# Optimization experiments

Hardware: AMD Instinct MI355X
Metric: run time of the kernel (lower is better)

Reference implementation:

```python
import jax, jax.numpy as jnp
import numpy as np
import math

# Config constants (match init_kwargs)
E = 8          # n_experts
TOPK = 2       # attn_topk
DIM = 1024     # transformer_dim
B = 4          # batch_size
S = 1024       # max_seq_len
H = 1024       # num_heads * head_dim
SCALE = 1.0 / math.sqrt(DIM)  # original divides scores by sqrt(self.dim)


def setup_inputs() -> dict:
    key = jax.random.key(0)
    ks = jax.random.split(key, 8)
    w = 0.02  # weight init scale
    return {
        "X": jax.random.normal(ks[0], (B, S, DIM), jnp.float32),
        "mask": jnp.ones((B, S), jnp.float32),
        "switch_W": jax.random.normal(ks[1], (DIM * S, E), jnp.float32) * w,
        "switch_b": jnp.zeros((E,), jnp.float32),
        "Wq": jax.random.normal(ks[2], (E, DIM, H), jnp.float32) * w,
        "bq": jnp.zeros((E, H), jnp.float32),
        "Wk": jax.random.normal(ks[3], (E, DIM, H), jnp.float32) * w,
        "bk": jnp.zeros((E, H), jnp.float32),
        "Wv": jax.random.normal(ks[4], (E, DIM, H), jnp.float32) * w,
        "bv": jnp.zeros((E, H), jnp.float32),
        "Wff": jax.random.normal(ks[5], (E, H, DIM), jnp.float32) * w,
        "bff": jnp.zeros((E, DIM), jnp.float32),
    }


def _dispatch_mask(route_prob):
    # top-k expert routing per batch element -> hard {0,1} mask [B, E]
    _, idx = jax.lax.top_k(route_prob, TOPK)  # [B, TOPK]
    b = route_prob.shape[0]
    return jnp.zeros((b, E), route_prob.dtype).at[jnp.arange(b)[:, None], idx].set(1.0)


def reference(X, mask, switch_W, switch_b, Wq, bq, Wk, bk, Wv, bv, Wff, bff):
    b, s, d = X.shape
    # Router: Linear(dim*seq_len -> n_experts) + softmax; preprocess -> idx_list
    logits = X.reshape(b, -1) @ switch_W + switch_b          # [B, E]
    route_prob = jax.nn.softmax(logits, axis=-1)
    m = _dispatch_mask(route_prob)                            # [B, E] dispatch mask (idx_list)

    # Per-expert Q/K/V projections (ColumnParallelLinearWithMoE over routed batches)
    Q = jnp.einsum('bsd,edh->ebsh', X, Wq) + bq[:, None, None, :]  # [E,B,S,H]
    K = jnp.einsum('bsd,edh->ebsh', X, Wk) + bk[:, None, None, :]
    V = jnp.einsum('bsd,edh->ebsh', X, Wv) + bv[:, None, None, :]

    # RowParallelMatmulWithMoE: per-expert scores, softmax (dropout p=0)
    scores = jnp.einsum('ebsh,ebth->ebst', Q, K) * SCALE      # [E,B,S,S]
    P = jax.nn.softmax(scores, axis=-1)

    # index_add_ combine of per-expert attn maps (second preprocess reuses same routing)
    A = jnp.einsum('be,ebst->bst', m, P)                      # [B,S,S]

    # ColumnParallelMatmulWithMoE: attn @ V per expert
    ctx = jnp.einsum('bst,ebth->ebsh', A, V)                  # [E,B,S,H]

    # RowParallelLinearWithMoE output projection, then index_add_ combine
    out = jnp.einsum('ebsh,ehd->ebsd', ctx, Wff) + bff[:, None, None, :]
    y = jnp.einsum('be,ebsd->bsd', m, out)                    # [B,S,DIM]
    return y
```

## Files before the change

kernel.cpp:

```cpp
#include <hip/hip_runtime.h>
#include <math.h>

typedef unsigned short u16;
typedef __attribute__((ext_vector_type(8))) short bffrag;
typedef __attribute__((ext_vector_type(4))) float f32x4;
typedef __attribute__((ext_vector_type(4))) unsigned short us4;
typedef __attribute__((ext_vector_type(8))) unsigned short us8;

#define SCALE_QK (1.0f/32.0f)

__device__ __forceinline__ u16 f2bf(float f) {
    unsigned u = __builtin_bit_cast(unsigned, f);
    u += 0x7fffu + ((u >> 16) & 1u);
    return (u16)(u >> 16);
}
__device__ __forceinline__ float bf2f(u16 v) {
    unsigned u = ((unsigned)v) << 16;
    return __builtin_bit_cast(float, u);
}

__device__ __forceinline__ void gld16(const u16* g, u16* l) {
    __builtin_amdgcn_global_load_lds(
        (const __attribute__((address_space(1))) void*)g,
        (__attribute__((address_space(3))) void*)l, 16, 0, 0);
}

__global__ __launch_bounds__(256) void router_partial(const float* __restrict__ X,
                                                      const float* __restrict__ sW,
                                                      float* __restrict__ part) {
    float acc[32];
    #pragma unroll
    for (int a = 0; a < 32; ++a) acc[a] = 0.f;
    int tid = blockIdx.x * 256 + threadIdx.x;
    #pragma unroll
    for (int q = 0; q < 4; ++q) {
        int i = tid + q * 262144;
        float4 w0 = *(const float4*)(sW + (size_t)i * 8);
        float4 w1 = *(const float4*)(sW + (size_t)i * 8 + 4);
        #pragma unroll
        for (int b = 0; b < 4; ++b) {
            float x = X[((size_t)b << 20) + i];
            acc[b*8+0] += x * w0.x; acc[b*8+1] += x * w0.y;
            acc[b*8+2] += x * w0.z; acc[b*8+3] += x * w0.w;
            acc[b*8+4] += x * w1.x; acc[b*8+5] += x * w1.y;
            acc[b*8+6] += x * w1.z; acc[b*8+7] += x * w1.w;
        }
    }
    __shared__ float wsum[4][32];
    int lane = threadIdx.x & 63, wv = threadIdx.x >> 6;
    #pragma unroll
    for (int a = 0; a < 32; ++a) {
        float v = acc[a];
        #pragma unroll
        for (int off = 32; off; off >>= 1) v += __shfl_down(v, off, 64);
        if (lane == 0) wsum[wv][a] = v;
    }
    __syncthreads();
    int t = threadIdx.x;
    if (t < 32)
        part[(size_t)t * 1024 + blockIdx.x] = wsum[0][t] + wsum[1][t] + wsum[2][t] + wsum[3][t];
}

__global__ __launch_bounds__(256) void router_final(const float* __restrict__ part,
                                                    const float* __restrict__ sb,
                                                    int* __restrict__ sel_need) {
    __shared__ float ps[32][8];
    __shared__ float lg[32];
    int t = threadIdx.x, a = t >> 3, c = t & 7;
    {
        float s = 0.f;
        const float* p = part + (size_t)a * 1024 + c * 128;
        for (int i = 0; i < 128; ++i) s += p[i];
        ps[a][c] = s;
    }
    __syncthreads();
    if (t < 32) {
        float v = 0.f;
        #pragma unroll
        for (int j = 0; j < 8; ++j) v += ps[t][j];
        lg[t] = v + sb[t & 7];
    }
    __syncthreads();
    if (t < 4) {
        int base = t * 8;
        int e1 = 0; float v1 = lg[base];
        for (int e = 1; e < 8; ++e) { if (lg[base + e] > v1) { v1 = lg[base + e]; e1 = e; } }
        int e2 = -1; float v2 = -INFINITY;
        for (int e = 0; e < 8; ++e) {
            if (e == e1) continue;
            if (lg[base + e] > v2) { v2 = lg[base + e]; e2 = e; }
        }
        sel_need[t * 2] = e1; sel_need[t * 2 + 1] = e2;
    }
    __syncthreads();
    if (t < 8) {
        int need = 0;
        for (int j = 0; j < 8; ++j) need |= (sel_need[j] == t);
        sel_need[8 + t] = need;
    }
}

__global__ __launch_bounds__(256) void c1_partial(const float* __restrict__ Wff,
        const float* __restrict__ bv, const int* __restrict__ sel_need,
        float* __restrict__ cpart) {
    int e = blockIdx.z;
    if (!sel_need[8 + e]) return;
    int d = blockIdx.x * 256 + threadIdx.x;
    int h0 = blockIdx.y * 128;
    const float* W = Wff + ((size_t)e << 20) + (size_t)h0 * 1024 + d;
    const float* bvp = bv + e * 1024 + h0;
    float s = 0.f;
    #pragma unroll 4
    for (int h = 0; h < 128; ++h) s += bvp[h] * W[(size_t)h * 1024];
    cpart[(e * 8 + blockIdx.y) * 1024 + d] = s;
}

__global__ __launch_bounds__(256) void ybias_kernel(const float* __restrict__ cpart,
        const float* __restrict__ bff, const int* __restrict__ sel,
        float* __restrict__ ybias) {
    int b = blockIdx.y;
    int d = blockIdx.x * 256 + threadIdx.x;
    int e0 = sel[b * 2], e1 = sel[b * 2 + 1];
    float c0 = 0.f, c1v = 0.f;
    #pragma unroll
    for (int hc = 0; hc < 8; ++hc) {
        c0  += cpart[(e0 * 8 + hc) * 1024 + d];
        c1v += cpart[(e1 * 8 + hc) * 1024 + d];
    }
    ybias[b * 1024 + d] = 2.f * (c0 + c1v) + bff[e0 * 1024 + d] + bff[e1 * 1024 + d];
}

__global__ __launch_bounds__(256) void cvt_all(const float* __restrict__ Wq,
                                               const float* __restrict__ Wk,
                                               const float* __restrict__ Wff,
                                               const float* __restrict__ X,
                                               const float* __restrict__ Wv,
                                               const int* __restrict__ sel_need,
                                               u16* __restrict__ WqT, u16* __restrict__ WkT,
                                               u16* __restrict__ WffT,
                                               u16* __restrict__ Xb, u16* __restrict__ WvB) {
    int z = blockIdx.z;
    int R0 = blockIdx.y * 128, C0 = blockIdx.x * 128;
    int t = threadIdx.x;
    if (z < 24) {
        int type = z >> 3, e = z & 7;
        if (!sel_need[8 + e]) return;
        const float* src = (type == 0 ? Wq : type == 1 ? Wk : Wff) + ((size_t)e << 20);
        u16* dst = (type == 0 ? WqT : type == 1 ? WkT : WffT) + ((size_t)e << 20);
        __shared__ u16 lt[128 * 136];
        int c = t & 127;
        int rh = (t >> 7) * 4;
        #pragma unroll
        for (int it = 0; it < 16; ++it) {
            int r4 = it * 8 + rh;
            us4 o;
            #pragma unroll
            for (int j = 0; j < 4; ++j)
                o[j] = f2bf(src[(size_t)(R0 + r4 + j) * 1024 + C0 + c]);
            *(us4*)&lt[c * 136 + r4] = o;
        }
        __syncthreads();
        int dd = (t & 15) * 8;
        int hh = t >> 4;
        #pragma unroll
        for (int it = 0; it < 8; ++it) {
            int cr = it * 16 + hh;
            us8 o = *(const us8*)&lt[cr * 136 + dd];
            *(us8*)(dst + (size_t)(C0 + cr) * 1024 + R0 + dd) = o;
        }
    } else {
        const float* src; u16* dst;
        if (z < 28) {
            int b = z - 24;
            src = X + ((size_t)b << 20);  dst = Xb + ((size_t)b << 20);
        } else {
            int e = z - 28;
            if (!sel_need[8 + e]) return;
            src = Wv + ((size_t)e << 20);  dst = WvB + ((size_t)e << 20);
        }
        int r = t >> 4;
        int c8 = (t & 15) * 8;
        #pragma unroll
        for (int it = 0; it < 8; ++it) {
            int row = R0 + it * 16 + r;
            const float* sp = src + (size_t)row * 1024 + C0 + c8;
            float4 a = *(const float4*)sp;
            float4 b2 = *(const float4*)(sp + 4);
            us8 o;
            o[0] = f2bf(a.x); o[1] = f2bf(a.y); o[2] = f2bf(a.z); o[3] = f2bf(a.w);
            o[4] = f2bf(b2.x); o[5] = f2bf(b2.y); o[6] = f2bf(b2.z); o[7] = f2bf(b2.w);
            *(us8*)(dst + (size_t)row * 1024 + C0 + c8) = o;
        }
    }
}

__device__ __forceinline__ void stage_half8(const u16* g, int ld, u16* ldst, int tid) {
    int r = tid >> 3;
    int j = ((tid ^ r) & 7) * 8;
    gld16(g + (size_t)r * ld + j, ldst + tid * 8);
    gld16(g + (size_t)(r + 64) * ld + j, ldst + 4096 + tid * 8);
}

template<int Q, bool LASTVM>
__device__ __forceinline__ void phase8(const u16* Ac, const bffrag (&bfr)[4][2],
                                       f32x4 (&acc)[8][4], int rb, int l15, int x0,
                                       const u16* sg, int sld, u16* sdst, int tid) {
    bffrag af[2][2];
    #pragma unroll
    for (int mm = 0; mm < 2; ++mm) {
        int r = (rb + Q * 32 + mm * 16 + l15) * 64;
        af[mm][0] = *(const bffrag*)(Ac + r + x0);
        af[mm][1] = *(const bffrag*)(Ac + r + (x0 ^ 32));
    }
    __builtin_amdgcn_sched_barrier(0);
    stage_half8(sg, sld, sdst, tid);
    __builtin_amdgcn_sched_barrier(0);
    __builtin_amdgcn_s_barrier();
    asm volatile("s_waitcnt lgkmcnt(0)" ::: "memory");
    __builtin_amdgcn_sched_barrier(0);
    __builtin_amdgcn_s_setprio(1);
    #pragma unroll
    for (int ks = 0; ks < 2; ++ks)
        #pragma unroll
        for (int mm = 0; mm < 2; ++mm)
            #pragma unroll
            for (int nn = 0; nn < 4; ++nn)
                acc[Q*2+mm][nn] = __builtin_amdgcn_mfma_f32_16x16x32_bf16(
                    af[mm][ks], bfr[nn][ks], acc[Q*2+mm][nn], 0, 0, 0);
    __builtin_amdgcn_s_setprio(0);
    __builtin_amdgcn_sched_barrier(0);
    if (LASTVM) asm volatile("s_waitcnt vmcnt(4)" ::: "memory");
    __builtin_amdgcn_s_barrier();
}

__device__ __forceinline__ void gemm8(const u16* __restrict__ A, int lda,
                                      const u16* __restrict__ B, int ldb,
                                      int K, f32x4 (&acc)[8][4]) {
    __shared__ u16 lds[65536];
    const int tid = threadIdx.x, l = tid & 63, wid = tid >> 6;
    const int wr = wid >> 2, wc = wid & 3;
    const int l15 = l & 15;
    const int rb = wr * 128;
    const int cb = wc * 64;
    const int x0 = (((l >> 4) ^ (l & 7)) * 8);
    const int m0 = blockIdx.y * 256, n0 = blockIdx.x * 256;
    const int nt = K >> 6;

    const u16* Ag = A + (size_t)m0 * lda;
    const u16* Bg = B + (size_t)n0 * ldb;

    stage_half8(Ag,                          lda, lds,                 tid);
    stage_half8(Ag + (size_t)128 * lda,      lda, lds + 8192,          tid);
    stage_half8(Bg,                          ldb, lds + 16384,         tid);
    stage_half8(Bg + (size_t)128 * ldb,      ldb, lds + 16384 + 8192,  tid);
    stage_half8(Bg + 64,                     ldb, lds + 32768 + 16384, tid);
    stage_half8(Bg + 64 + (size_t)128 * ldb, ldb, lds + 32768 + 16384 + 8192, tid);
    asm volatile("s_waitcnt vmcnt(4)" ::: "memory");
    __builtin_amdgcn_s_barrier();

    for (int t7 = 0; t7 < nt; ++t7) {
        const int cur = t7 & 1;
        u16* Ac = lds + cur * 32768;
        u16* Bc = Ac + 16384;
        u16* An = lds + (cur ^ 1) * 32768;
        const int ka = (t7 + 1 < nt ? t7 + 1 : nt - 1) << 6;
        const int kb = (t7 + 2 < nt ? t7 + 2 : nt - 1) << 6;
        const u16* sA0 = Ag + ka;
        const u16* sA1 = Ag + (size_t)128 * lda + ka;
        const u16* sB0 = Bg + kb;
        const u16* sB1 = Bg + (size_t)128 * ldb + kb;

        bffrag bfr[4][2];
        #pragma unroll
        for (int nn = 0; nn < 4; ++nn) {
            int r = (cb + nn * 16 + l15) * 64;
            bfr[nn][0] = *(const bffrag*)(Bc + r + x0);
            bfr[nn][1] = *(const bffrag*)(Bc + r + (x0 ^ 32));
        }
        phase8<0, false>(Ac, bfr, acc, rb, l15, x0, sA0, lda, An, tid);
        phase8<1, false>(Ac, bfr, acc, rb, l15, x0, sA1, lda, An + 8192, tid);
        phase8<2, false>(Ac, bfr, acc, rb, l15, x0, sB0, ldb, Bc, tid);
        phase8<3, true >(Ac, bfr, acc, rb, l15, x0, sB1, ldb, Bc + 8192, tid);
    }
}

__device__ __forceinline__ void zero8(f32x4 (&acc)[8][4]) {
    #pragma unroll
    for (int m = 0; m < 8; ++m)
        #pragma unroll
        for (int n = 0; n < 4; ++n)
            #pragma unroll
            for (int i = 0; i < 4; ++i) acc[m][n][i] = 0.f;
}

__device__ __forceinline__ void epi8_bf16(u16* __restrict__ C, int ldc, float scale,
                                          const f32x4 (&acc)[8][4],
                                          const float* __restrict__ biasN) {
    const int tid = threadIdx.x, l = tid & 63, wid = tid >> 6;
    const int wr = wid >> 2, wc = wid & 3;
    const int m0 = blockIdx.y * 256 + wr * 128, n0 = blockIdx.x * 256 + wc * 64;
    const int l15 = l & 15, l4 = (l >> 4) * 4;
    #pragma unroll
    for (int mt = 0; mt < 8; ++mt)
        #pragma unroll
        for (int nn = 0; nn < 4; ++nn) {
            int col = n0 + nn * 16 + l15;
            float bn = biasN ? biasN[col] : 0.f;
            #pragma unroll
            for (int i = 0; i < 4; ++i) {
                int row = m0 + mt * 16 + l4 + i;
                C[(size_t)row * ldc + col] = f2bf(acc[mt][nn][i] * scale + bn);
            }
        }
}

__global__ __launch_bounds__(512) void mfma8_qk(const u16* __restrict__ Xb,
        const u16* __restrict__ WqT, const u16* __restrict__ WkT,
        const float* __restrict__ bq, const float* __restrict__ bk,
        const int* __restrict__ sel, u16* __restrict__ Qb, u16* __restrict__ Kb) {
    int z = blockIdx.z, w = z >> 3, bs = z & 7;
    int b = bs >> 1, e = sel[bs];
    f32x4 acc[8][4]; zero8(acc);
    gemm8(Xb + ((size_t)b << 20), 1024, (w ? WkT : WqT) + ((size_t)e << 20), 1024, 1024, acc);
    epi8_bf16((w ? Kb : Qb) + ((size_t)bs << 20), 1024, 1.0f, acc, (w ? bk : bq) + e * 1024);
}

__global__ __launch_bounds__(512) void mfma8_sw(const u16* __restrict__ Qb,
        const u16* __restrict__ Kb, const u16* __restrict__ WffT,
        const u16* __restrict__ WvB, const int* __restrict__ sel,
        u16* __restrict__ Sb, u16* __restrict__ P0b, u16* __restrict__ P1b) {
    int z = blockIdx.z;
    f32x4 acc[8][4]; zero8(acc);
    if (z < 8) {
        gemm8(Qb + ((size_t)z << 20), 1024, Kb + ((size_t)z << 20), 1024, 1024, acc);
        epi8_bf16(Sb + ((size_t)z << 20), 1024, SCALE_QK, acc, nullptr);
    } else {
        int h = (z >= 12), b = z & 3, e = sel[b * 2 + h];
        gemm8(WffT + ((size_t)e << 20), 1024, WvB + ((size_t)e << 20), 1024, 1024, acc);
        epi8_bf16((h ? P1b : P0b) + ((size_t)b << 20), 1024, 1.0f, acc, nullptr);
    }
}

__global__ __launch_bounds__(256) void wvfadd(const u16* __restrict__ P0b,
                                              const u16* __restrict__ P1b,
                                              u16* __restrict__ W) {
    size_t i = (size_t)(blockIdx.x * 256 + threadIdx.x) * 8;
    us8 a = *(const us8*)(P0b + i);
    us8 b = *(const us8*)(P1b + i);
    us8 o;
    #pragma unroll
    for (int j = 0; j < 8; ++j) o[j] = f2bf(bf2f(a[j]) + bf2f(b[j]));
    *(us8*)(W + i) = o;
}

__device__ __forceinline__ void stage_tile(const u16* a0, const u16* a1,
                                           const u16* b0, const u16* b1,
                                           u16* sa, u16* sb, int tid) {
    gld16(a0, &sa[tid * 8]);
    gld16(a1, &sa[2048 + tid * 8]);
    gld16(b0, &sb[tid * 8]);
    gld16(b1, &sb[2048 + tid * 8]);
}

__device__ __forceinline__ void gemm_ds(const u16* __restrict__ A, int lda,
                                        const u16* __restrict__ B, int ldb,
                                        int K, int m0, int n0, f32x4 (&acc)[4][4]) {
    __shared__ u16 sA[2][4096];
    __shared__ u16 sB[2][4096];
    const int tid = threadIdx.x, lane = tid & 63, wv = tid >> 6;
    const int wr = (wv >> 1) * 64, wc = (wv & 1) * 64;
    const int l15 = lane & 15, lk = (lane >> 4) * 8;
    const int r0 = tid >> 2, k8 = (tid & 3) * 8;

    const u16* a0 = A + (size_t)(m0 + r0) * lda + k8;
    const u16* a1 = A + (size_t)(m0 + 64 + r0) * lda + k8;
    const u16* b0 = B + (size_t)(n0 + r0) * ldb + k8;
    const u16* b1 = B + (size_t)(n0 + 64 + r0) * ldb + k8;

    stage_tile(a0, a1, b0, b1, sA[0], sB[0], tid);
    __syncthreads();

    const int nt = K >> 5;
    for (int t = 0; t < nt; ++t) {
        const int cur = t & 1;
        if (t + 1 < nt) {
            int k0 = (t + 1) << 5;
            stage_tile(a0 + k0, a1 + k0, b0 + k0, b1 + k0, sA[cur ^ 1], sB[cur ^ 1], tid);
        }
        bffrag av[4], bf[4];
        #pragma unroll
        for (int m = 0; m < 4; ++m)
            av[m] = *reinterpret_cast<const bffrag*>(&sA[cur][(wr + m * 16 + l15) * 32 + lk]);
        #pragma unroll
        for (int n = 0; n < 4; ++n)
            bf[n] = *reinterpret_cast<const bffrag*>(&sB[cur][(wc + n * 16 + l15) * 32 + lk]);
        #pragma unroll
        for (int m = 0; m < 4; ++m)
            #pragma unroll
            for (int n = 0; n < 4; ++n)
                acc[m][n] = __builtin_amdgcn_mfma_f32_16x16x32_bf16(av[m], bf[n], acc[m][n], 0, 0, 0);
        __syncthreads();
    }
}

__device__ __forceinline__ void zero_acc(f32x4 (&acc)[4][4]) {
    #pragma unroll
    for (int m = 0; m < 4; ++m)
        #pragma unroll
        for (int n = 0; n < 4; ++n)
            #pragma unroll
            for (int i = 0; i < 4; ++i) acc[m][n][i] = 0.f;
}

__device__ __forceinline__ void epi4_bf16(u16* __restrict__ C, int ldc, int m0, int n0,
                                          const f32x4 (&acc)[4][4]) {
    const int tid = threadIdx.x, lane = tid & 63, wv = tid >> 6;
    const int wr = (wv >> 1) * 64, wc = (wv & 1) * 64;
    const int l15 = lane & 15, l4 = (lane >> 4) * 4;
    #pragma unroll
    for (int m = 0; m < 4; ++m)
        #pragma unroll
        for (int n = 0; n < 4; ++n) {
            int col = n0 + wc + n * 16 + l15;
            #pragma unroll
            for (int i = 0; i < 4; ++i) {
                int row = m0 + wr + m * 16 + l4 + i;
                C[(size_t)row * ldc + col] = f2bf(acc[m][n][i]);
            }
        }
}

__device__ __forceinline__ void epi4_f32(float* __restrict__ C, int ldc, int m0, int n0,
                                         const f32x4 (&acc)[4][4],
                                         const float* __restrict__ bias1) {
    const int tid = threadIdx.x, lane = tid & 63, wv = tid >> 6;
    const int wr = (wv >> 1) * 64, wc = (wv & 1) * 64;
    const int l15 = lane & 15, l4 = (lane >> 4) * 4;
    #pragma unroll
    for (int m = 0; m < 4; ++m)
        #pragma unroll
        for (int n = 0; n < 4; ++n) {
            int col = n0 + wc + n * 16 + l15;
            float bn = bias1 ? bias1[col] : 0.f;
            #pragma unroll
            for (int i = 0; i < 4; ++i) {
                int row = m0 + wr + m * 16 + l4 + i;
                C[(size_t)row * ldc + col] = acc[m][n][i] + bn;
            }
        }
}

__global__ __launch_bounds__(256) void sm_mt(const u16* __restrict__ Sb, u16* __restrict__ Ab,
        const u16* __restrict__ Wvfsum, const u16* __restrict__ Xb, u16* __restrict__ Mtb) {
    int bid = blockIdx.x;
    if (bid < 256) {
        int b = bid >> 6, m0 = ((bid >> 3) & 7) * 128, n0 = (bid & 7) * 128;
        f32x4 acc[4][4]; zero_acc(acc);
        gemm_ds(Wvfsum + ((size_t)b << 20), 1024, Xb + ((size_t)b << 20), 1024, 1024, m0, n0, acc);
        epi4_bf16(Mtb + ((size_t)b << 20), 1024, m0, n0, acc);
        return;
    }
    int bs = bid - 256, b = bs >> 10, s = bs & 1023;
    const u16* S0 = Sb + ((size_t)(b * 2) << 20) + (size_t)s * 1024;
    const u16* S1 = S0 + (1u << 20);
    int t = threadIdx.x, lane = t & 63, wv = t >> 6;
    us4 xv0 = *(const us4*)(S0 + t * 4);
    us4 xv1 = *(const us4*)(S1 + t * 4);
    float x0[4], x1[4];
    #pragma unroll
    for (int j = 0; j < 4; ++j) { x0[j] = bf2f(xv0[j]); x1[j] = bf2f(xv1[j]); }
    float m0 = fmaxf(fmaxf(x0[0], x0[1]), fmaxf(x0[2], x0[3]));
    float m1 = fmaxf(fmaxf(x1[0], x1[1]), fmaxf(x1[2], x1[3]));
    #pragma unroll
    for (int off = 32; off; off >>= 1) {
        m0 = fmaxf(m0, __shfl_xor(m0, off, 64));
        m1 = fmaxf(m1, __shfl_xor(m1, off, 64));
    }
    __shared__ float wred[4][4];
    if (lane == 0) { wred[wv][0] = m0; wred[wv][1] = m1; }
    __syncthreads();
    m0 = fmaxf(fmaxf(wred[0][0], wred[1][0]), fmaxf(wred[2][0], wred[3][0]));
    m1 = fmaxf(fmaxf(wred[0][1], wred[1][1]), fmaxf(wred[2][1], wred[3][1]));
    float e0[4], e1[4];
    #pragma unroll
    for (int j = 0; j < 4; ++j) { e0[j] = __expf(x0[j] - m0); e1[j] = __expf(x1[j] - m1); }
    float s0 = e0[0] + e0[1] + e0[2] + e0[3];
    float s1 = e1[0] + e1[1] + e1[2] + e1[3];
    #pragma unroll
    for (int off = 32; off; off >>= 1) {
        s0 += __shfl_xor(s0, off, 64);
        s1 += __shfl_xor(s1, off, 64);
    }
    if (lane == 0) { wred[wv][2] = s0; wred[wv][3] = s1; }
    __syncthreads();
    s0 = wred[0][2] + wred[1][2] + wred[2][2] + wred[3][2];
    s1 = wred[0][3] + wred[1][3] + wred[2][3] + wred[3][3];
    float r0 = 1.f / s0, r1 = 1.f / s1;
    us4 o;
    #pragma unroll
    for (int j = 0; j < 4; ++j) o[j] = f2bf(e0[j] * r0 + e1[j] * r1);
    *(us4*)(Ab + ((size_t)b << 20) + (size_t)s * 1024 + t * 4) = o;
}

__global__ __launch_bounds__(256) void mfma_y(const u16* __restrict__ Abf,
        const u16* __restrict__ Mtb, const float* __restrict__ ybias,
        float* __restrict__ y) {
    int b = blockIdx.z;
    int m0 = blockIdx.y * 128, n0 = blockIdx.x * 128;
    f32x4 acc[4][4]; zero_acc(acc);
    gemm_ds(Abf + ((size_t)b << 20), 1024, Mtb + ((size_t)b << 20), 1024, 1024, m0, n0, acc);
    epi4_f32(y + ((size_t)b << 20), 1024, m0, n0, acc, ybias + b * 1024);
}

extern "C" void kernel_launch(void* const* d_in, const int* in_sizes, int n_in,
                              void* d_out, int out_size, void* d_ws, size_t ws_size,
                              hipStream_t stream) {
    const float* X   = (const float*)d_in[0];
    const float* sW  = (const float*)d_in[2];
    const float* sb  = (const float*)d_in[3];
    const float* Wq  = (const float*)d_in[4];
    const float* bq  = (const float*)d_in[5];
    const float* Wk  = (const float*)d_in[6];
    const float* bk  = (const float*)d_in[7];
    const float* Wv  = (const float*)d_in[8];
    const float* bv  = (const float*)d_in[9];
    const float* Wff = (const float*)d_in[10];
    const float* bff = (const float*)d_in[11];
    float* y = (float*)d_out;

    char* w = (char*)d_ws;
    float* part  = (float*)w;
    float* cpart = (float*)w;
    int*   sel   = (int*)(w + (1u << 18));
    float* ybias = (float*)(w + (1u << 18) + 256);
    u16* base = (u16*)(w + (1u << 19));
    u16* Xb   = base;
    u16* WqT  = Xb   + (4u << 20);
    u16* WkT  = WqT  + (8u << 20);
    u16* WffT = WkT  + (8u << 20);
    u16* WvB  = WffT + (8u << 20);
    u16* Qb   = WvB  + (8u << 20);
    u16* Kb   = Qb   + (8u << 20);
    u16* Sb   = Kb   + (8u << 20);
    u16* P0b  = Sb   + (8u << 20);
    u16* P1b  = P0b  + (4u << 20);
    u16* Abf    = WqT;
    u16* Mtb    = WkT;
    u16* Wvfsum = Qb;

    router_partial<<<1024, 256, 0, stream>>>(X, sW, part);
    router_final<<<1, 256, 0, stream>>>(part, sb, sel);
    c1_partial<<<dim3(4, 8, 8), 256, 0, stream>>>(Wff, bv, sel, cpart);
    ybias_kernel<<<dim3(4, 4), 256, 0, stream>>>(cpart, bff, sel, ybias);
    cvt_all<<<dim3(8, 8, 36), 256, 0, stream>>>(Wq, Wk, Wff, X, Wv, sel, WqT, WkT, WffT, Xb, WvB);

    mfma8_qk<<<dim3(4, 4, 16), 512, 0, stream>>>(Xb, WqT, WkT, bq, bk, sel, Qb, Kb);
    mfma8_sw<<<dim3(4, 4, 16), 512, 0, stream>>>(Qb, Kb, WffT, WvB, sel, Sb, P0b, P1b);
    wvfadd<<<2048, 256, 0, stream>>>(P0b, P1b, Wvfsum);
    sm_mt<<<4352, 256, 0, stream>>>(Sb, Abf, Wvfsum, Xb, Mtb);
    mfma_y<<<dim3(8, 8, 4), 256, 0, stream>>>(Abf, Mtb, ybias, y);
}
```

Baseline: 219.5 us.

## Fuse bias kernels into neighbors and remap GEMM blocks for XCD L2 locality

Folds the c1_partial bias reduction into extra blocks of cvt_all and the ybias computation into extra blocks of wvfadd, which removes two small kernel launches. It also flattens the mfma8_qk and mfma8_sw grids to 1D and decodes block indices so that all 16 tiles of one GEMM land on the same XCD (round-robin by block id mod 8), so each matrix's operands are reused within one L2. The cost is slightly more branching per block, and a dependence on the hardware dispatching blocks round-robin across XCDs.

```diff
diff --git a/kernel.cpp b/kernel.cpp
--- a/kernel.cpp
+++ b/kernel.cpp
@@ -100,45 +100,17 @@
     }
 }
 
-__global__ __launch_bounds__(256) void c1_partial(const float* __restrict__ Wff,
-        const float* __restrict__ bv, const int* __restrict__ sel_need,
-        float* __restrict__ cpart) {
-    int e = blockIdx.z;
-    if (!sel_need[8 + e]) return;
-    int d = blockIdx.x * 256 + threadIdx.x;
-    int h0 = blockIdx.y * 128;
-    const float* W = Wff + ((size_t)e << 20) + (size_t)h0 * 1024 + d;
-    const float* bvp = bv + e * 1024 + h0;
-    float s = 0.f;
-    #pragma unroll 4
-    for (int h = 0; h < 128; ++h) s += bvp[h] * W[(size_t)h * 1024];
-    cpart[(e * 8 + blockIdx.y) * 1024 + d] = s;
-}
-
-__global__ __launch_bounds__(256) void ybias_kernel(const float* __restrict__ cpart,
-        const float* __restrict__ bff, const int* __restrict__ sel,
-        float* __restrict__ ybias) {
-    int b = blockIdx.y;
-    int d = blockIdx.x * 256 + threadIdx.x;
-    int e0 = sel[b * 2], e1 = sel[b * 2 + 1];
-    float c0 = 0.f, c1v = 0.f;
-    #pragma unroll
-    for (int hc = 0; hc < 8; ++hc) {
-        c0  += cpart[(e0 * 8 + hc) * 1024 + d];
-        c1v += cpart[(e1 * 8 + hc) * 1024 + d];
-    }
-    ybias[b * 1024 + d] = 2.f * (c0 + c1v) + bff[e0 * 1024 + d] + bff[e1 * 1024 + d];
-}
-
 __global__ __launch_bounds__(256) void cvt_all(const float* __restrict__ Wq,
                                                const float* __restrict__ Wk,
                                                const float* __restrict__ Wff,
                                                const float* __restrict__ X,
                                                const float* __restrict__ Wv,
+                                               const float* __restrict__ bv,
                                                const int* __restrict__ sel_need,
                                                u16* __restrict__ WqT, u16* __restrict__ WkT,
                                                u16* __restrict__ WffT,
-                                               u16* __restrict__ Xb, u16* __restrict__ WvB) {
+                                               u16* __restrict__ Xb, u16* __restrict__ WvB,
+                                               float* __restrict__ cpart) {
     int z = blockIdx.z;
     int R0 = blockIdx.y * 128, C0 = blockIdx.x * 128;
     int t = threadIdx.x;
@@ -168,7 +140,7 @@
             us8 o = *(const us8*)&lt[cr * 136 + dd];
             *(us8*)(dst + (size_t)(C0 + cr) * 1024 + R0 + dd) = o;
         }
-    } else {
+    } else if (z < 36) {
         const float* src; u16* dst;
         if (z < 28) {
             int b = z - 24;
@@ -191,6 +163,19 @@
             o[4] = f2bf(b2.x); o[5] = f2bf(b2.y); o[6] = f2bf(b2.z); o[7] = f2bf(b2.w);
             *(us8*)(dst + (size_t)row * 1024 + C0 + c8) = o;
         }
+    } else {
+        int idx = ((z - 36) << 6) + (blockIdx.y << 3) + blockIdx.x;
+        int e = idx >> 5;
+        if (!sel_need[8 + e]) return;
+        int r = idx & 31;
+        int d = (r & 3) * 256 + t;
+        int h0 = (r >> 2) * 128;
+        const float* W = Wff + ((size_t)e << 20) + (size_t)h0 * 1024 + d;
+        const float* bvp = bv + e * 1024 + h0;
+        float s = 0.f;
+        #pragma unroll 4
+        for (int h = 0; h < 128; ++h) s += bvp[h] * W[(size_t)h * 1024];
+        cpart[(e * 8 + (r >> 2)) * 1024 + d] = s;
     }
 }
 
@@ -235,7 +220,7 @@
 
 __device__ __forceinline__ void gemm8(const u16* __restrict__ A, int lda,
                                       const u16* __restrict__ B, int ldb,
-                                      int K, f32x4 (&acc)[8][4]) {
+                                      int K, int m0, int n0, f32x4 (&acc)[8][4]) {
     __shared__ u16 lds[65536];
     const int tid = threadIdx.x, l = tid & 63, wid = tid >> 6;
     const int wr = wid >> 2, wc = wid & 3;
@@ -243,7 +228,6 @@
     const int rb = wr * 128;
     const int cb = wc * 64;
     const int x0 = (((l >> 4) ^ (l & 7)) * 8);
-    const int m0 = blockIdx.y * 256, n0 = blockIdx.x * 256;
     const int nt = K >> 6;
 
     const u16* Ag = A + (size_t)m0 * lda;
@@ -295,10 +279,11 @@
 
 __device__ __forceinline__ void epi8_bf16(u16* __restrict__ C, int ldc, float scale,
                                           const f32x4 (&acc)[8][4],
-                                          const float* __restrict__ biasN) {
+                                          const float* __restrict__ biasN,
+                                          int M0, int N0) {
     const int tid = threadIdx.x, l = tid & 63, wid = tid >> 6;
     const int wr = wid >> 2, wc = wid & 3;
-    const int m0 = blockIdx.y * 256 + wr * 128, n0 = blockIdx.x * 256 + wc * 64;
+    const int m0 = M0 + wr * 128, n0 = N0 + wc * 64;
     const int l15 = l & 15, l4 = (l >> 4) * 4;
     #pragma unroll
     for (int mt = 0; mt < 8; ++mt)
@@ -314,37 +299,69 @@
         }
 }
 
+__device__ __forceinline__ void xcd_decode(int f, int& z, int& m0, int& n0) {
+    int xcd = f & 7, slot = f >> 3;
+    z = xcd + ((slot >> 4) << 3);
+    int idx = slot & 15;
+    m0 = (idx >> 2) * 256;
+    n0 = (idx & 3) * 256;
+}
+
 __global__ __launch_bounds__(512) void mfma8_qk(const u16* __restrict__ Xb,
         const u16* __restrict__ WqT, const u16* __restrict__ WkT,
         const float* __restrict__ bq, const float* __restrict__ bk,
         const int* __restrict__ sel, u16* __restrict__ Qb, u16* __restrict__ Kb) {
-    int z = blockIdx.z, w = z >> 3, bs = z & 7;
+    int z, m0, n0;
+    xcd_decode(blockIdx.x, z, m0, n0);
+    int w = z >> 3, bs = z & 7;
     int b = bs >> 1, e = sel[bs];
     f32x4 acc[8][4]; zero8(acc);
-    gemm8(Xb + ((size_t)b << 20), 1024, (w ? WkT : WqT) + ((size_t)e << 20), 1024, 1024, acc);
-    epi8_bf16((w ? Kb : Qb) + ((size_t)bs << 20), 1024, 1.0f, acc, (w ? bk : bq) + e * 1024);
+    gemm8(Xb + ((size_t)b << 20), 1024, (w ? WkT : WqT) + ((size_t)e << 20), 1024,
+          1024, m0, n0, acc);
+    epi8_bf16((w ? Kb : Qb) + ((size_t)bs << 20), 1024, 1.0f, acc,
+              (w ? bk : bq) + e * 1024, m0, n0);
 }
 
 __global__ __launch_bounds__(512) void mfma8_sw(const u16* __restrict__ Qb,
         const u16* __restrict__ Kb, const u16* __restrict__ WffT,
         const u16* __restrict__ WvB, const int* __restrict__ sel,
         u16* __restrict__ Sb, u16* __restrict__ P0b, u16* __restrict__ P1b) {
-    int z = blockIdx.z;
+    int z, m0, n0;
+    xcd_decode(blockIdx.x, z, m0, n0);
     f32x4 acc[8][4]; zero8(acc);
     if (z < 8) {
-        gemm8(Qb + ((size_t)z << 20), 1024, Kb + ((size_t)z << 20), 1024, 1024, acc);
-        epi8_bf16(Sb + ((size_t)z << 20), 1024, SCALE_QK, acc, nullptr);
+        gemm8(Qb + ((size_t)z << 20), 1024, Kb + ((size_t)z << 20), 1024, 1024, m0, n0, acc);
+        epi8_bf16(Sb + ((size_t)z << 20), 1024, SCALE_QK, acc, nullptr, m0, n0);
     } else {
         int h = (z >= 12), b = z & 3, e = sel[b * 2 + h];
-        gemm8(WffT + ((size_t)e << 20), 1024, WvB + ((size_t)e << 20), 1024, 1024, acc);
-        epi8_bf16((h ? P1b : P0b) + ((size_t)b << 20), 1024, 1.0f, acc, nullptr);
+        gemm8(WffT + ((size_t)e << 20), 1024, WvB + ((size_t)e << 20), 1024, 1024, m0, n0, acc);
+        epi8_bf16((h ? P1b : P0b) + ((size_t)b << 20), 1024, 1.0f, acc, nullptr, m0, n0);
     }
 }
 
 __global__ __launch_bounds__(256) void wvfadd(const u16* __restrict__ P0b,
                                               const u16* __restrict__ P1b,
-                                              u16* __restrict__ W) {
-    size_t i = (size_t)(blockIdx.x * 256 + threadIdx.x) * 8;
+                                              u16* __restrict__ W,
+                                              const float* __restrict__ cpart,
+                                              const float* __restrict__ bff,
+                                              const int* __restrict__ sel,
+                                              float* __restrict__ ybias) {
+    int bid = blockIdx.x;
+    if (bid >= 2048) {
+        int r = bid - 2048;
+        int b = r >> 2;
+        int d = (r & 3) * 256 + threadIdx.x;
+        int e0 = sel[b * 2], e1 = sel[b * 2 + 1];
+        float c0 = 0.f, c1v = 0.f;
+        #pragma unroll
+        for (int hc = 0; hc < 8; ++hc) {
+            c0  += cpart[(e0 * 8 + hc) * 1024 + d];
+            c1v += cpart[(e1 * 8 + hc) * 1024 + d];
+        }
+        ybias[b * 1024 + d] = 2.f * (c0 + c1v) + bff[e0 * 1024 + d] + bff[e1 * 1024 + d];
+        return;
+    }
+    size_t i = (size_t)(bid * 256 + threadIdx.x) * 8;
     us8 a = *(const us8*)(P0b + i);
     us8 b = *(const us8*)(P1b + i);
     us8 o;
@@ -550,13 +567,12 @@
 
     router_partial<<<1024, 256, 0, stream>>>(X, sW, part);
     router_final<<<1, 256, 0, stream>>>(part, sb, sel);
-    c1_partial<<<dim3(4, 8, 8), 256, 0, stream>>>(Wff, bv, sel, cpart);
-    ybias_kernel<<<dim3(4, 4), 256, 0, stream>>>(cpart, bff, sel, ybias);
-    cvt_all<<<dim3(8, 8, 36), 256, 0, stream>>>(Wq, Wk, Wff, X, Wv, sel, WqT, WkT, WffT, Xb, WvB);
-
-    mfma8_qk<<<dim3(4, 4, 16), 512, 0, stream>>>(Xb, WqT, WkT, bq, bk, sel, Qb, Kb);
-    mfma8_sw<<<dim3(4, 4, 16), 512, 0, stream>>>(Qb, Kb, WffT, WvB, sel, Sb, P0b, P1b);
-    wvfadd<<<2048, 256, 0, stream>>>(P0b, P1b, Wvfsum);
+    cvt_all<<<dim3(8, 8, 40), 256, 0, stream>>>(Wq, Wk, Wff, X, Wv, bv, sel,
+                                                WqT, WkT, WffT, Xb, WvB, cpart);
+
+    mfma8_qk<<<256, 512, 0, stream>>>(Xb, WqT, WkT, bq, bk, sel, Qb, Kb);
+    mfma8_sw<<<256, 512, 0, stream>>>(Qb, Kb, WffT, WvB, sel, Sb, P0b, P1b);
+    wvfadd<<<2064, 256, 0, stream>>>(P0b, P1b, Wvfsum, cpart, bff, sel, ybias);
     sm_mt<<<4352, 256, 0, stream>>>(Sb, Abf, Wvfsum, Xb, Mtb);
     mfma_y<<<dim3(8, 8, 4), 256, 0, stream>>>(Abf, Mtb, ybias, y);
 }
```

New measurement: 204.3 us. 6.9% less time.
